# Performance work log

Measured on AMD Instinct MI355X. Metric: run time of the kernel, lower is better.

Reference implementation:

```python
import jax, jax.numpy as jnp
import numpy as np

L, DIN, D, NL = 16384, 256, 768, 8
EPS = 1e-5


def _ln(x, g, b):
    mu = jnp.mean(x, axis=-1, keepdims=True)
    var = jnp.mean(jnp.square(x - mu), axis=-1, keepdims=True)
    return (x - mu) * jax.lax.rsqrt(var + EPS) * g + b


def setup_inputs() -> dict:
    key = jax.random.key(0)
    ks = iter(jax.random.split(key, 24))
    nrm = lambda shape, s=0.02: jax.random.normal(next(ks), shape, jnp.float32) * s
    return {
        "node_features": jax.random.normal(next(ks), (L, DIN), jnp.float32),
        "W_proj": nrm((DIN, D)), "b_proj": jnp.zeros((D,), jnp.float32),
        "ln_s_g": jnp.ones((NL, D), jnp.float32), "ln_s_b": jnp.zeros((NL, D), jnp.float32),
        "W_in": nrm((NL, D, D)), "b_in": jnp.zeros((NL, D), jnp.float32),
        "W_gate": nrm((NL, D, D)), "b_gate": jnp.zeros((NL, D), jnp.float32),
        "W_out": nrm((NL, D, D)), "b_out": jnp.zeros((NL, D), jnp.float32),
        "decay_logit": nrm((NL, D), 0.5),
        "ln_f_g": jnp.ones((NL, D), jnp.float32), "ln_f_b": jnp.zeros((NL, D), jnp.float32),
        "W_ff1": nrm((NL, D, 2 * D)), "b_ff1": jnp.zeros((NL, 2 * D), jnp.float32),
        "W_ff2": nrm((NL, 2 * D, D)), "b_ff2": jnp.zeros((NL, D), jnp.float32),
        "ln_o_g": jnp.ones((D,), jnp.float32), "ln_o_b": jnp.zeros((D,), jnp.float32),
    }


def reference(node_features, W_proj, b_proj, ln_s_g, ln_s_b, W_in, b_in,
              W_gate, b_gate, W_out, b_out, decay_logit, ln_f_g, ln_f_b,
              W_ff1, b_ff1, W_ff2, b_ff2, ln_o_g, ln_o_b):
    x = node_features @ W_proj + b_proj  # [L, D]
    for l in range(NL):
        h = _ln(x, ln_s_g[l], ln_s_b[l])
        u = h @ W_in[l] + b_in[l]                      # [L, D]
        gate = jax.nn.sigmoid(h @ W_gate[l] + b_gate[l])
        decay = jax.nn.sigmoid(decay_logit[l])         # [D]

        def step(state, u_t):
            state = decay * state + u_t
            return state, state

        _, states = jax.lax.scan(step, jnp.zeros((D,), x.dtype), u)  # [L, D]
        x = x + (states * gate) @ W_out[l] + b_out[l]
        hf = _ln(x, ln_f_g[l], ln_f_b[l])
        x = x + jax.nn.silu(hf @ W_ff1[l] + b_ff1[l]) @ W_ff2[l] + b_ff2[l]
    return _ln(x, ln_o_g, ln_o_b)
```

## Files before the change

kernel.cpp:

```cpp
#include <hip/hip_runtime.h>
#include <hip/hip_bf16.h>
#include <math.h>
#include <string.h>

#define L_TOK 16384
#define D_INP 256
#define D_MOD 768
#define D_FF  1536
#define N_LAYER 8
#define S_T 64
#define S_G 256
#define EPSV 1e-5f

typedef short bf16x8 __attribute__((ext_vector_type(8)));
typedef float f32x4 __attribute__((ext_vector_type(4)));
typedef __hip_bfloat16 bf16;
typedef unsigned int u32;
typedef unsigned short u16;

__device__ __forceinline__ float fsigmoid(float z) { return 1.0f / (1.0f + __expf(-z)); }

__device__ __forceinline__ u16 f2bf(float f) {
  __hip_bfloat16 h = __float2bfloat16(f);
  u16 r; memcpy(&r, &h, 2); return r;
}
__device__ __forceinline__ float bf2f(u16 v) {
  u32 x = ((u32)v) << 16; float f; memcpy(&f, &x, 4); return f;
}

__device__ __forceinline__ void glds16(const short* g, short* l) {
  __builtin_amdgcn_global_load_lds(
      (const __attribute__((address_space(1))) unsigned int*)(g),
      (__attribute__((address_space(3))) unsigned int*)(l), 16, 0, 0);
}

__global__ void k_f32_to_bf16v(const float4* __restrict__ src, ushort4* __restrict__ dst, int n4) {
  int i = blockIdx.x * blockDim.x + threadIdx.x;
  if (i < n4) {
    float4 v = src[i];
    ushort4 o; o.x = f2bf(v.x); o.y = f2bf(v.y); o.z = f2bf(v.z); o.w = f2bf(v.w);
    dst[i] = o;
  }
}

template<bool FOLD>
__global__ void k_transpose_fold(const float* __restrict__ src, bf16* __restrict__ dst,
                                 int R, int C, size_t sstride, size_t dstride,
                                 const float* __restrict__ gv, const float* __restrict__ bv,
                                 float* __restrict__ wacc, float* __restrict__ bacc,
                                 int vstride) {
  __shared__ float tile[32][33];
  int z = blockIdx.z;
  const float* s = src + (size_t)z * sstride;
  bf16* d = dst + (size_t)z * dstride;
  int r0 = blockIdx.y * 32, c0 = blockIdx.x * 32;
  int tx = threadIdx.x, ty = threadIdx.y;
#pragma unroll
  for (int i = ty; i < 32; i += 8)
    tile[i][tx] = s[(size_t)(r0 + i) * C + (c0 + tx)];
  __syncthreads();
  float gk = 1.0f;
  if (FOLD) gk = gv[(size_t)z * R + r0 + tx];
#pragma unroll
  for (int i = ty; i < 32; i += 8) {
    float val = tile[tx][i];
    if (FOLD) val *= gk;
    d[(size_t)(c0 + i) * R + (r0 + tx)] = __float2bfloat16(val);
  }
  if (FOLD && ty == 0) {
    const float* gz = gv + (size_t)z * R + r0;
    const float* bz = bv + (size_t)z * R + r0;
    float s1 = 0.f, s2 = 0.f;
#pragma unroll 8
    for (int j = 0; j < 32; j++) {
      float wv = tile[j][tx];
      s1 += gz[j] * wv;
      s2 += bz[j] * wv;
    }
    atomicAdd(&wacc[(size_t)z * vstride + c0 + tx], s1);
    atomicAdd(&bacc[(size_t)z * vstride + c0 + tx], s2);
  }
}

template<int MODE, bool LNFOLD, bool STATS>
__global__ __launch_bounds__(256, 4) void k_gemm128(
    const short* __restrict__ A, const short* __restrict__ Bt,
    const float* __restrict__ bias, const float* __restrict__ bias2,
    const float* __restrict__ wvec, const float* __restrict__ bvec,
    const float* __restrict__ stats_in, float* __restrict__ stats_out,
    u16* __restrict__ res, u16* __restrict__ outp, u16* __restrict__ outp2,
    int N, int K, int ncol)
{
  __shared__ short As[2][128 * 32];
  __shared__ short Bs[2][128 * 32];
  __shared__ float s_mu[128], s_rv[128];
  const int tid = threadIdx.x;
  const int lane = tid & 63, w = tid >> 6;
  const int wr = w >> 1, wc = w & 1;
  const int l16 = lane & 15, qd = lane >> 4;

  const int b = blockIdx.x;
  const int xcd = b & 7, t = b >> 3;
  const int m0 = (xcd * 16 + t / ncol) * 128;
  const int n0 = (t % ncol) * 128;

  const int sr = lane >> 2, sc = lane & 3;
  const int ar = w * 32 + sr;
  const int acx = sc ^ ((ar >> 1) & 3);
  const short* ag0 = A  + (size_t)(m0 + ar) * K + acx * 8;
  const short* ag1 = ag0 + (size_t)16 * K;
  const short* bg0 = Bt + (size_t)(n0 + ar) * K + acx * 8;
  const short* bg1 = bg0 + (size_t)16 * K;

  const int fo = (qd ^ ((l16 >> 1) & 3)) * 8 + l16 * 32;

  f32x4 acc[4][4];
#pragma unroll
  for (int i = 0; i < 4; i++)
#pragma unroll
    for (int j = 0; j < 4; j++) acc[i][j] = (f32x4){0.f, 0.f, 0.f, 0.f};

  {
    short* a0 = &As[0][w * 1024];
    glds16(ag0, a0); glds16(ag1, a0 + 512);
    short* b0 = &Bs[0][w * 1024];
    glds16(bg0, b0); glds16(bg1, b0 + 512);
  }
  if (LNFOLD && tid < 128) {
    float sv  = stats_in[2 * (m0 + tid)];
    float sq  = stats_in[2 * (m0 + tid) + 1];
    float mu  = sv * (1.0f / (float)D_MOD);
    float var = sq * (1.0f / (float)D_MOD) - mu * mu;
    s_mu[tid] = mu;
    s_rv[tid] = 1.0f / sqrtf(var + EPSV);
  }
  int p = 0;
  for (int k0 = 0; k0 < K; k0 += 32, p ^= 1) {
    __syncthreads();
    if (k0 + 32 < K) {
      short* a0 = &As[p ^ 1][w * 1024];
      glds16(ag0 + k0 + 32, a0); glds16(ag1 + k0 + 32, a0 + 512);
      short* b0 = &Bs[p ^ 1][w * 1024];
      glds16(bg0 + k0 + 32, b0); glds16(bg1 + k0 + 32, b0 + 512);
    }
    const short* afb = &As[p][wr * 2048 + fo];
    const short* bfb = &Bs[p][wc * 2048 + fo];
    bf16x8 af[4], bfr[4];
#pragma unroll
    for (int rt = 0; rt < 4; rt++) af[rt] = *(const bf16x8*)(afb + rt * 512);
#pragma unroll
    for (int ct = 0; ct < 4; ct++) bfr[ct] = *(const bf16x8*)(bfb + ct * 512);
#pragma unroll
    for (int rt = 0; rt < 4; rt++)
#pragma unroll
      for (int ct = 0; ct < 4; ct++)
        acc[rt][ct] = __builtin_amdgcn_mfma_f32_16x16x32_bf16(af[rt], bfr[ct], acc[rt][ct], 0, 0, 0);
  }

  const float* bb = bias;
  u16* op = outp;
  int nofs = 0, Nout = N;
  bool sig = false;
  if (MODE == 4) {
    Nout = N >> 1;
    if (n0 >= Nout) { bb = bias2; op = outp2; nofs = Nout; sig = true; }
  }
  const int gmb = m0 + wr * 64 + qd * 4;
  const int gnb = n0 + wc * 64 + l16;
  float bc[4], wv4[4], bv4[4];
#pragma unroll
  for (int ct = 0; ct < 4; ct++) {
    int gn = gnb + ct * 16;
    bc[ct] = bb[gn - nofs];
    if (LNFOLD) { wv4[ct] = wvec[gn]; bv4[ct] = bvec[gn]; }
  }
#pragma unroll
  for (int rt = 0; rt < 4; rt++) {
#pragma unroll
    for (int r = 0; r < 4; r++) {
      const int gm = gmb + rt * 16 + r;
      float mu = 0.f, rv = 0.f;
      if (LNFOLD) { mu = s_mu[gm - m0]; rv = s_rv[gm - m0]; }
      float ps = 0.f, ps2 = 0.f;
#pragma unroll
      for (int ct = 0; ct < 4; ct++) {
        int gn = gnb + ct * 16;
        float vv = acc[rt][ct][r];
        if (LNFOLD) vv = rv * vv - rv * mu * wv4[ct] + bv4[ct] + bc[ct];
        else        vv += bc[ct];
        if (MODE == 2) vv = vv * fsigmoid(vv);
        if (MODE == 4 && sig) vv = fsigmoid(vv);
        size_t oidx = (size_t)gm * Nout + (gn - nofs);
        if (MODE == 3) vv += bf2f(res[oidx]);
        u16 rb = f2bf(vv);
        op[oidx] = rb;
        if (STATS) { float fv = bf2f(rb); ps += fv; ps2 += fv * fv; }
      }
      if (STATS) {
#pragma unroll
        for (int o = 1; o < 16; o <<= 1) {
          ps  += __shfl_xor(ps, o, 64);
          ps2 += __shfl_xor(ps2, o, 64);
        }
        if (l16 == 0) {
          atomicAdd(&stats_out[2 * gm], ps);
          atomicAdd(&stats_out[2 * gm + 1], ps2);
        }
      }
    }
  }
}

__global__ void k_scan_a(const bf16* __restrict__ u, const float* __restrict__ dl,
                         float* __restrict__ clast) {
  int t = threadIdx.x;
  int g = blockIdx.x;
  int d0 = t * 4;
  float dec[4], s[4] = {0.f, 0.f, 0.f, 0.f};
#pragma unroll
  for (int c = 0; c < 4; c++) dec[c] = fsigmoid(dl[d0 + c]);
  const ushort4* up = (const ushort4*)(u + (size_t)g * S_T * D_MOD) + t;
  for (int tt = 0; tt < S_T; tt++) {
    ushort4 uv = up[(size_t)tt * 192];
    s[0] = fmaf(dec[0], s[0], bf2f(uv.x));
    s[1] = fmaf(dec[1], s[1], bf2f(uv.y));
    s[2] = fmaf(dec[2], s[2], bf2f(uv.z));
    s[3] = fmaf(dec[3], s[3], bf2f(uv.w));
  }
#pragma unroll
  for (int c = 0; c < 4; c++) clast[(size_t)g * D_MOD + d0 + c] = s[c];
}

__global__ void k_scan_b(const float* __restrict__ clast, const float* __restrict__ dl,
                         float* __restrict__ carry) {
  int d = threadIdx.x;
  float decay = fsigmoid(dl[d]);
  float aT = decay;
#pragma unroll
  for (int i = 0; i < 6; i++) aT *= aT;
  float c = 0.f;
  for (int g = 0; g < S_G; g++) {
    carry[(size_t)g * D_MOD + d] = c;
    c = fmaf(aT, c, clast[(size_t)g * D_MOD + d]);
  }
}

__global__ void k_scan_c(const bf16* __restrict__ u, const float* __restrict__ dl,
                         const float* __restrict__ carry, bf16* __restrict__ gate_s) {
  int t = threadIdx.x;
  int g = blockIdx.x;
  int d0 = t * 4;
  float dec[4], s[4];
#pragma unroll
  for (int c = 0; c < 4; c++) {
    dec[c] = fsigmoid(dl[d0 + c]);
    s[c] = carry[(size_t)g * D_MOD + d0 + c];
  }
  const ushort4* up = (const ushort4*)(u + (size_t)g * S_T * D_MOD) + t;
  ushort4* gp = (ushort4*)(gate_s + (size_t)g * S_T * D_MOD) + t;
  for (int tt = 0; tt < S_T; tt++) {
    ushort4 uv = up[(size_t)tt * 192];
    ushort4 gv = gp[(size_t)tt * 192];
    s[0] = fmaf(dec[0], s[0], bf2f(uv.x));
    s[1] = fmaf(dec[1], s[1], bf2f(uv.y));
    s[2] = fmaf(dec[2], s[2], bf2f(uv.z));
    s[3] = fmaf(dec[3], s[3], bf2f(uv.w));
    ushort4 ov;
    ov.x = f2bf(s[0] * bf2f(gv.x));
    ov.y = f2bf(s[1] * bf2f(gv.y));
    ov.z = f2bf(s[2] * bf2f(gv.z));
    ov.w = f2bf(s[3] * bf2f(gv.w));
    gp[(size_t)tt * 192] = ov;
  }
}

__global__ __launch_bounds__(256) void k_ln_final(const u16* __restrict__ x,
    const float* __restrict__ stats, const float* __restrict__ g,
    const float* __restrict__ b, float* __restrict__ outp) {
  int wv = threadIdx.x >> 6, lane = threadIdx.x & 63;
  int row = blockIdx.x * 4 + wv;
  float sv = stats[2 * row], sq = stats[2 * row + 1];
  float mu = sv * (1.0f / (float)D_MOD);
  float var = sq * (1.0f / (float)D_MOD) - mu * mu;
  float rv = 1.0f / sqrtf(var + EPSV);
  const ushort4* xr = (const ushort4*)(x + (size_t)row * D_MOD);
  const float4* g4 = (const float4*)g;
  const float4* b4 = (const float4*)b;
  float4* o4 = (float4*)(outp + (size_t)row * D_MOD);
#pragma unroll
  for (int j = 0; j < 3; j++) {
    int f = j * 64 + lane;
    ushort4 xv = xr[f];
    float4 gg = g4[f], bb = b4[f], ov;
    ov.x = (bf2f(xv.x) - mu) * rv * gg.x + bb.x;
    ov.y = (bf2f(xv.y) - mu) * rv * gg.y + bb.y;
    ov.z = (bf2f(xv.z) - mu) * rv * gg.z + bb.z;
    ov.w = (bf2f(xv.w) - mu) * rv * gg.w + bb.w;
    o4[f] = ov;
  }
}

extern "C" void kernel_launch(void* const* d_in, const int* in_sizes, int n_in,
                              void* d_out, int out_size, void* d_ws, size_t ws_size,
                              hipStream_t stream) {
  const float* nf     = (const float*)d_in[0];
  const float* W_proj = (const float*)d_in[1];
  const float* b_proj = (const float*)d_in[2];
  const float* ln_s_g = (const float*)d_in[3];
  const float* ln_s_b = (const float*)d_in[4];
  const float* W_in   = (const float*)d_in[5];
  const float* b_in   = (const float*)d_in[6];
  const float* W_gate = (const float*)d_in[7];
  const float* b_gate = (const float*)d_in[8];
  const float* W_out  = (const float*)d_in[9];
  const float* b_out  = (const float*)d_in[10];
  const float* dlogit = (const float*)d_in[11];
  const float* ln_f_g = (const float*)d_in[12];
  const float* ln_f_b = (const float*)d_in[13];
  const float* W_ff1  = (const float*)d_in[14];
  const float* b_ff1  = (const float*)d_in[15];
  const float* W_ff2  = (const float*)d_in[16];
  const float* b_ff2  = (const float*)d_in[17];
  const float* ln_o_g = (const float*)d_in[18];
  const float* ln_o_b = (const float*)d_in[19];
  (void)in_sizes; (void)n_in;

  char* ws = (char*)d_ws;
  size_t off = 0;
  auto alloc = [&](size_t bytes) -> char* {
    char* p = ws + off;
    off = (off + bytes + 255) & ~(size_t)255;
    return p;
  };
  const bool big = ws_size >= (160ull << 20);
  const size_t wmul = big ? N_LAYER : 1;

  u16*   x     = (u16*)alloc(2ull * L_TOK * D_MOD);
  char*  ug    = alloc(2ull * L_TOK * D_FF);
  u16*   u     = (u16*)ug;
  u16*   gate  = (u16*)(ug + 2ull * L_TOK * D_MOD);
  u16*   tb    = (u16*)ug;
  u16*   nfb   = (u16*)ug;
  bf16*  WprojT= (bf16*)alloc(2ull * D_INP * D_MOD);
  bf16*  WigT  = (bf16*)alloc(2ull * wmul * (2 * D_MOD) * D_MOD);
  bf16*  WoT   = (bf16*)alloc(2ull * wmul * D_MOD * D_MOD);
  bf16*  Wff1T = (bf16*)alloc(2ull * wmul * D_MOD * D_FF);
  bf16*  Wff2T = (bf16*)alloc(2ull * wmul * D_FF * D_MOD);
  float* clast = (float*)alloc(sizeof(float) * (size_t)S_G * D_MOD);
  float* carry = (float*)alloc(sizeof(float) * (size_t)S_G * D_MOD);
  char*  zbase = alloc(0);
  float* stats = (float*)alloc(sizeof(float) * 17ull * L_TOK * 2);
  float* wvig  = (float*)alloc(sizeof(float) * N_LAYER * 2 * D_MOD);
  float* bvig  = (float*)alloc(sizeof(float) * N_LAYER * 2 * D_MOD);
  float* wvf1  = (float*)alloc(sizeof(float) * N_LAYER * D_FF);
  float* bvf1  = (float*)alloc(sizeof(float) * N_LAYER * D_FF);
  size_t zbytes = (size_t)((char*)ws + off - zbase);
  hipMemsetAsync(zbase, 0, zbytes, stream);

  const size_t DD = (size_t)D_MOD * D_MOD, DF = (size_t)D_MOD * D_FF;
  auto statslot = [&](int s) { return stats + (size_t)s * L_TOK * 2; };
  dim3 tb32(32, 8);
  k_f32_to_bf16v<<<(L_TOK * D_INP / 4 + 255) / 256, 256, 0, stream>>>(
      (const float4*)nf, (ushort4*)nfb, L_TOK * D_INP / 4);
  k_transpose_fold<false><<<dim3(D_MOD / 32, D_INP / 32, 1), tb32, 0, stream>>>(
      W_proj, WprojT, D_INP, D_MOD, 0, 0, nullptr, nullptr, nullptr, nullptr, 0);
  if (big) {
    k_transpose_fold<true><<<dim3(D_MOD / 32, D_MOD / 32, N_LAYER), tb32, 0, stream>>>(
        W_in,   WigT,      D_MOD, D_MOD, DD, 2 * DD, ln_s_g, ln_s_b, wvig,       bvig,       2 * D_MOD);
    k_transpose_fold<true><<<dim3(D_MOD / 32, D_MOD / 32, N_LAYER), tb32, 0, stream>>>(
        W_gate, WigT + DD, D_MOD, D_MOD, DD, 2 * DD, ln_s_g, ln_s_b, wvig + D_MOD, bvig + D_MOD, 2 * D_MOD);
    k_transpose_fold<false><<<dim3(D_MOD / 32, D_MOD / 32, N_LAYER), tb32, 0, stream>>>(
        W_out,  WoT,       D_MOD, D_MOD, DD, DD, nullptr, nullptr, nullptr, nullptr, 0);
    k_transpose_fold<true><<<dim3(D_FF / 32,  D_MOD / 32, N_LAYER), tb32, 0, stream>>>(
        W_ff1,  Wff1T,     D_MOD, D_FF,  DF, DF, ln_f_g, ln_f_b, wvf1, bvf1, D_FF);
    k_transpose_fold<false><<<dim3(D_MOD / 32, D_FF / 32,  N_LAYER), tb32, 0, stream>>>(
        W_ff2,  Wff2T,     D_FF,  D_MOD, DF, DF, nullptr, nullptr, nullptr, nullptr, 0);
  }

  k_gemm128<0, false, true><<<128 * 6, 256, 0, stream>>>(
      (const short*)nfb, (const short*)WprojT, b_proj, nullptr, nullptr, nullptr,
      nullptr, statslot(0), nullptr, x, nullptr, D_MOD, D_INP, 6);

  for (int l = 0; l < N_LAYER; l++) {
    const bf16 *wigT, *woT, *wf1T, *wf2T;
    if (big) {
      wigT = WigT  + (size_t)l * 2 * DD;
      woT  = WoT   + (size_t)l * DD;
      wf1T = Wff1T + (size_t)l * DF;
      wf2T = Wff2T + (size_t)l * DF;
    } else {
      k_transpose_fold<true><<<dim3(D_MOD / 32, D_MOD / 32, 1), tb32, 0, stream>>>(
          W_in + (size_t)l * DD, WigT, D_MOD, D_MOD, 0, 0,
          ln_s_g + l * D_MOD, ln_s_b + l * D_MOD, wvig + (size_t)l * 2 * D_MOD, bvig + (size_t)l * 2 * D_MOD, 0);
      k_transpose_fold<true><<<dim3(D_MOD / 32, D_MOD / 32, 1), tb32, 0, stream>>>(
          W_gate + (size_t)l * DD, WigT + DD, D_MOD, D_MOD, 0, 0,
          ln_s_g + l * D_MOD, ln_s_b + l * D_MOD, wvig + (size_t)l * 2 * D_MOD + D_MOD, bvig + (size_t)l * 2 * D_MOD + D_MOD, 0);
      k_transpose_fold<false><<<dim3(D_MOD / 32, D_MOD / 32, 1), tb32, 0, stream>>>(
          W_out + (size_t)l * DD, WoT, D_MOD, D_MOD, 0, 0, nullptr, nullptr, nullptr, nullptr, 0);
      k_transpose_fold<true><<<dim3(D_FF / 32, D_MOD / 32, 1), tb32, 0, stream>>>(
          W_ff1 + (size_t)l * DF, Wff1T, D_MOD, D_FF, 0, 0,
          ln_f_g + l * D_MOD, ln_f_b + l * D_MOD, wvf1 + (size_t)l * D_FF, bvf1 + (size_t)l * D_FF, 0);
      k_transpose_fold<false><<<dim3(D_MOD / 32, D_FF / 32, 1), tb32, 0, stream>>>(
          W_ff2 + (size_t)l * DF, Wff2T, D_FF, D_MOD, 0, 0, nullptr, nullptr, nullptr, nullptr, 0);
      wigT = WigT; woT = WoT; wf1T = Wff1T; wf2T = Wff2T;
    }

    k_gemm128<4, true, false><<<128 * 12, 256, 0, stream>>>(
        (const short*)x, (const short*)wigT, b_in + l * D_MOD, b_gate + l * D_MOD,
        wvig + (size_t)l * 2 * D_MOD, bvig + (size_t)l * 2 * D_MOD,
        statslot(2 * l), nullptr, nullptr, u, gate, 2 * D_MOD, D_MOD, 12);
    k_scan_a<<<S_G, 192, 0, stream>>>((const bf16*)u, dlogit + l * D_MOD, clast);
    k_scan_b<<<1, D_MOD, 0, stream>>>(clast, dlogit + l * D_MOD, carry);
    k_scan_c<<<S_G, 192, 0, stream>>>((const bf16*)u, dlogit + l * D_MOD, carry, (bf16*)gate);
    k_gemm128<3, false, true><<<128 * 6, 256, 0, stream>>>(
        (const short*)gate, (const short*)woT, b_out + l * D_MOD, nullptr, nullptr, nullptr,
        nullptr, statslot(2 * l + 1), x, x, nullptr, D_MOD, D_MOD, 6);
    k_gemm128<2, true, false><<<128 * 12, 256, 0, stream>>>(
        (const short*)x, (const short*)wf1T, b_ff1 + l * D_FF, nullptr,
        wvf1 + (size_t)l * D_FF, bvf1 + (size_t)l * D_FF,
        statslot(2 * l + 1), nullptr, nullptr, tb, nullptr, D_FF, D_MOD, 12);
    k_gemm128<3, false, true><<<128 * 6, 256, 0, stream>>>(
        (const short*)tb, (const short*)wf2T, b_ff2 + l * D_MOD, nullptr, nullptr, nullptr,
        nullptr, statslot(2 * l + 2), x, x, nullptr, D_MOD, D_FF, 6);
  }

  k_ln_final<<<L_TOK / 4, 256, 0, stream>>>(x, statslot(2 * N_LAYER), ln_o_g, ln_o_b, (float*)d_out);
}
```

Measured before the change: 2.290 ms.

## Replace 128x128 GEMM with 256x256 tile, 8-wave ping-pong pipelined kernel

```diff
diff --git a/kernel.cpp b/kernel.cpp
--- a/kernel.cpp
+++ b/kernel.cpp
@@ -83,7 +83,7 @@
 }
 
 template<int MODE, bool LNFOLD, bool STATS>
-__global__ __launch_bounds__(256, 4) void k_gemm128(
+__global__ __launch_bounds__(512, 2) void k_gemm256(
     const short* __restrict__ A, const short* __restrict__ Bt,
     const float* __restrict__ bias, const float* __restrict__ bias2,
     const float* __restrict__ wvec, const float* __restrict__ bvec,
@@ -91,70 +91,133 @@
     u16* __restrict__ res, u16* __restrict__ outp, u16* __restrict__ outp2,
     int N, int K, int ncol)
 {
-  __shared__ short As[2][128 * 32];
-  __shared__ short Bs[2][128 * 32];
-  __shared__ float s_mu[128], s_rv[128];
+  __shared__ short As[4 * 8192];
+  __shared__ short Bs[4 * 8192];
+  __shared__ float s_mu[256], s_rv[256];
+
   const int tid = threadIdx.x;
   const int lane = tid & 63, w = tid >> 6;
-  const int wr = w >> 1, wc = w & 1;
+  const int wr = w >> 2, wc = w & 3;
   const int l16 = lane & 15, qd = lane >> 4;
 
   const int b = blockIdx.x;
-  const int xcd = b & 7, t = b >> 3;
-  const int m0 = (xcd * 16 + t / ncol) * 128;
-  const int n0 = (t % ncol) * 128;
-
-  const int sr = lane >> 2, sc = lane & 3;
-  const int ar = w * 32 + sr;
-  const int acx = sc ^ ((ar >> 1) & 3);
-  const short* ag0 = A  + (size_t)(m0 + ar) * K + acx * 8;
-  const short* ag1 = ag0 + (size_t)16 * K;
-  const short* bg0 = Bt + (size_t)(n0 + ar) * K + acx * 8;
-  const short* bg1 = bg0 + (size_t)16 * K;
-
-  const int fo = (qd ^ ((l16 >> 1) & 3)) * 8 + l16 * 32;
-
-  f32x4 acc[4][4];
-#pragma unroll
-  for (int i = 0; i < 4; i++)
-#pragma unroll
-    for (int j = 0; j < 4; j++) acc[i][j] = (f32x4){0.f, 0.f, 0.f, 0.f};
-
-  {
-    short* a0 = &As[0][w * 1024];
-    glds16(ag0, a0); glds16(ag1, a0 + 512);
-    short* b0 = &Bs[0][w * 1024];
-    glds16(bg0, b0); glds16(bg1, b0 + 512);
-  }
-  if (LNFOLD && tid < 128) {
-    float sv  = stats_in[2 * (m0 + tid)];
-    float sq  = stats_in[2 * (m0 + tid) + 1];
+  const int xcd = b & 7, tt = b >> 3;
+  const int m0 = (xcd * 8 + tt / ncol) * 256;
+  const int n0 = (tt % ncol) * 256;
+
+  const int srow  = w * 16 + (lane >> 2);
+  const int skoct = (lane & 3) ^ ((lane >> 3) & 3);
+  const short* pA0 = A  + (size_t)(m0 + srow) * K + skoct * 8;
+  const short* pA1 = pA0 + (size_t)128 * K;
+  const short* pB0 = Bt + (size_t)(n0 + srow) * K + skoct * 8;
+  const short* pB1 = pB0 + (size_t)128 * K;
+
+  auto stg = [&](short* region, const short* p0, const short* p1, int koff) {
+    glds16(p0 + koff, region + w * 512);
+    glds16(p1 + koff, region + 4096 + w * 512);
+  };
+
+  const int kx   = (qd ^ ((l16 >> 1) & 3)) << 4;
+  const int aoff = (wr * 128 + l16) * 64 + kx;
+  const int boff = (wc * 64  + l16) * 64 + kx;
+
+  float sv = 0.f, sq = 0.f;
+  if (LNFOLD && tid < 256) {
+    sv = stats_in[2 * (m0 + tid)];
+    sq = stats_in[2 * (m0 + tid) + 1];
+  }
+
+  const int NT = K >> 6;
+  stg(Bs + 0 * 8192, pB0, pB1, 0);
+  stg(As + 0 * 8192, pA0, pA1, 0);
+  stg(Bs + 1 * 8192, pB0, pB1, 32);
+  stg(As + 1 * 8192, pA0, pA1, 32);
+  stg(Bs + 2 * 8192, pB0, pB1, 64);
+  stg(As + 2 * 8192, pA0, pA1, 64);
+  stg(Bs + 3 * 8192, pB0, pB1, 96);
+
+  if (LNFOLD && tid < 256) {
     float mu  = sv * (1.0f / (float)D_MOD);
     float var = sq * (1.0f / (float)D_MOD) - mu * mu;
     s_mu[tid] = mu;
     s_rv[tid] = 1.0f / sqrtf(var + EPSV);
   }
-  int p = 0;
-  for (int k0 = 0; k0 < K; k0 += 32, p ^= 1) {
-    __syncthreads();
-    if (k0 + 32 < K) {
-      short* a0 = &As[p ^ 1][w * 1024];
-      glds16(ag0 + k0 + 32, a0); glds16(ag1 + k0 + 32, a0 + 512);
-      short* b0 = &Bs[p ^ 1][w * 1024];
-      glds16(bg0 + k0 + 32, b0); glds16(bg1 + k0 + 32, b0 + 512);
-    }
-    const short* afb = &As[p][wr * 2048 + fo];
-    const short* bfb = &Bs[p][wc * 2048 + fo];
-    bf16x8 af[4], bfr[4];
-#pragma unroll
-    for (int rt = 0; rt < 4; rt++) af[rt] = *(const bf16x8*)(afb + rt * 512);
-#pragma unroll
-    for (int ct = 0; ct < 4; ct++) bfr[ct] = *(const bf16x8*)(bfb + ct * 512);
-#pragma unroll
-    for (int rt = 0; rt < 4; rt++)
-#pragma unroll
-      for (int ct = 0; ct < 4; ct++)
-        acc[rt][ct] = __builtin_amdgcn_mfma_f32_16x16x32_bf16(af[rt], bfr[ct], acc[rt][ct], 0, 0, 0);
+
+  f32x4 acc[8][4];
+#pragma unroll
+  for (int i = 0; i < 8; i++)
+#pragma unroll
+    for (int j = 0; j < 4; j++) acc[i][j] = (f32x4){0.f, 0.f, 0.f, 0.f};
+
+  asm volatile("s_waitcnt vmcnt(6)" ::: "memory");
+  __builtin_amdgcn_s_barrier();
+
+  bf16x8 af[4], b0f[4], b1f[4];
+  int buf = 0;
+  for (int t = 0; t < NT; ++t, buf ^= 1) {
+    const char* Ak0 = (const char*)As + buf * 32768;
+    const char* Ak1 = Ak0 + 16384;
+    const char* Bk0 = (const char*)Bs + buf * 32768;
+    const char* Bk1 = Bk0 + 16384;
+    const int nb = buf ^ 1;
+
+    if (t + 1 < NT) stg(As + (nb * 2 + 1) * 8192, pA0, pA1, (t + 1) * 64 + 32);
+#pragma unroll
+    for (int i = 0; i < 4; i++) af[i]  = *(const bf16x8*)(Ak0 + aoff + i * 1024);
+#pragma unroll
+    for (int i = 0; i < 4; i++) b0f[i] = *(const bf16x8*)(Bk0 + boff + i * 1024);
+    __builtin_amdgcn_s_barrier();
+    __builtin_amdgcn_s_setprio(1);
+#pragma unroll
+    for (int rf = 0; rf < 4; rf++)
+#pragma unroll
+      for (int cf = 0; cf < 4; cf++)
+        acc[rf][cf] = __builtin_amdgcn_mfma_f32_16x16x32_bf16(af[rf], b0f[cf], acc[rf][cf], 0, 0, 0);
+    __builtin_amdgcn_s_setprio(0);
+    __builtin_amdgcn_s_barrier();
+
+    if (t + 2 < NT) stg(Bs + (buf * 2 + 0) * 8192, pB0, pB1, (t + 2) * 64);
+#pragma unroll
+    for (int i = 0; i < 4; i++) af[i] = *(const bf16x8*)(Ak0 + aoff + (4 + i) * 1024);
+    __builtin_amdgcn_s_barrier();
+    __builtin_amdgcn_s_setprio(1);
+#pragma unroll
+    for (int rf = 0; rf < 4; rf++)
+#pragma unroll
+      for (int cf = 0; cf < 4; cf++)
+        acc[4 + rf][cf] = __builtin_amdgcn_mfma_f32_16x16x32_bf16(af[rf], b0f[cf], acc[4 + rf][cf], 0, 0, 0);
+    __builtin_amdgcn_s_setprio(0);
+    __builtin_amdgcn_s_barrier();
+
+    if (t + 2 < NT) stg(As + (buf * 2 + 0) * 8192, pA0, pA1, (t + 2) * 64);
+#pragma unroll
+    for (int i = 0; i < 4; i++) af[i]  = *(const bf16x8*)(Ak1 + aoff + i * 1024);
+#pragma unroll
+    for (int i = 0; i < 4; i++) b1f[i] = *(const bf16x8*)(Bk1 + boff + i * 1024);
+    __builtin_amdgcn_s_barrier();
+    __builtin_amdgcn_s_setprio(1);
+#pragma unroll
+    for (int rf = 0; rf < 4; rf++)
+#pragma unroll
+      for (int cf = 0; cf < 4; cf++)
+        acc[rf][cf] = __builtin_amdgcn_mfma_f32_16x16x32_bf16(af[rf], b1f[cf], acc[rf][cf], 0, 0, 0);
+    __builtin_amdgcn_s_setprio(0);
+    __builtin_amdgcn_s_barrier();
+
+    if (t + 2 < NT) stg(Bs + (buf * 2 + 1) * 8192, pB0, pB1, (t + 2) * 64 + 32);
+#pragma unroll
+    for (int i = 0; i < 4; i++) af[i] = *(const bf16x8*)(Ak1 + aoff + (4 + i) * 1024);
+    __builtin_amdgcn_s_barrier();
+    __builtin_amdgcn_s_setprio(1);
+#pragma unroll
+    for (int rf = 0; rf < 4; rf++)
+#pragma unroll
+      for (int cf = 0; cf < 4; cf++)
+        acc[4 + rf][cf] = __builtin_amdgcn_mfma_f32_16x16x32_bf16(af[rf], b1f[cf], acc[4 + rf][cf], 0, 0, 0);
+    __builtin_amdgcn_s_setprio(0);
+    if (t + 2 < NT) asm volatile("s_waitcnt vmcnt(6)" ::: "memory");
+    else            asm volatile("s_waitcnt vmcnt(0)" ::: "memory");
+    __builtin_amdgcn_s_barrier();
   }
 
   const float* bb = bias;
@@ -165,29 +228,29 @@
     Nout = N >> 1;
     if (n0 >= Nout) { bb = bias2; op = outp2; nofs = Nout; sig = true; }
   }
-  const int gmb = m0 + wr * 64 + qd * 4;
+  const int gmb = m0 + wr * 128 + qd * 4;
   const int gnb = n0 + wc * 64 + l16;
   float bc[4], wv4[4], bv4[4];
 #pragma unroll
-  for (int ct = 0; ct < 4; ct++) {
-    int gn = gnb + ct * 16;
-    bc[ct] = bb[gn - nofs];
-    if (LNFOLD) { wv4[ct] = wvec[gn]; bv4[ct] = bvec[gn]; }
-  }
-#pragma unroll
-  for (int rt = 0; rt < 4; rt++) {
+  for (int cf = 0; cf < 4; cf++) {
+    int gn = gnb + cf * 16;
+    bc[cf] = bb[gn - nofs];
+    if (LNFOLD) { wv4[cf] = wvec[gn]; bv4[cf] = bvec[gn]; }
+  }
+#pragma unroll
+  for (int rf = 0; rf < 8; rf++) {
 #pragma unroll
     for (int r = 0; r < 4; r++) {
-      const int gm = gmb + rt * 16 + r;
+      const int gm = gmb + rf * 16 + r;
       float mu = 0.f, rv = 0.f;
       if (LNFOLD) { mu = s_mu[gm - m0]; rv = s_rv[gm - m0]; }
       float ps = 0.f, ps2 = 0.f;
 #pragma unroll
-      for (int ct = 0; ct < 4; ct++) {
-        int gn = gnb + ct * 16;
-        float vv = acc[rt][ct][r];
-        if (LNFOLD) vv = rv * vv - rv * mu * wv4[ct] + bv4[ct] + bc[ct];
-        else        vv += bc[ct];
+      for (int cf = 0; cf < 4; cf++) {
+        int gn = gnb + cf * 16;
+        float vv = acc[rf][cf][r];
+        if (LNFOLD) vv = rv * vv - rv * mu * wv4[cf] + bv4[cf] + bc[cf];
+        else        vv += bc[cf];
         if (MODE == 2) vv = vv * fsigmoid(vv);
         if (MODE == 4 && sig) vv = fsigmoid(vv);
         size_t oidx = (size_t)gm * Nout + (gn - nofs);
@@ -377,9 +440,9 @@
         W_ff2,  Wff2T,     D_FF,  D_MOD, DF, DF, nullptr, nullptr, nullptr, nullptr, 0);
   }
 
-  k_gemm128<0, false, true><<<128 * 6, 256, 0, stream>>>(
+  k_gemm256<0, false, true><<<64 * 3, 512, 0, stream>>>(
       (const short*)nfb, (const short*)WprojT, b_proj, nullptr, nullptr, nullptr,
-      nullptr, statslot(0), nullptr, x, nullptr, D_MOD, D_INP, 6);
+      nullptr, statslot(0), nullptr, x, nullptr, D_MOD, D_INP, 3);
 
   for (int l = 0; l < N_LAYER; l++) {
     const bf16 *wigT, *woT, *wf1T, *wf2T;
@@ -405,23 +468,23 @@
       wigT = WigT; woT = WoT; wf1T = Wff1T; wf2T = Wff2T;
     }
 
-    k_gemm128<4, true, false><<<128 * 12, 256, 0, stream>>>(
+    k_gemm256<4, true, false><<<64 * 6, 512, 0, stream>>>(
         (const short*)x, (const short*)wigT, b_in + l * D_MOD, b_gate + l * D_MOD,
         wvig + (size_t)l * 2 * D_MOD, bvig + (size_t)l * 2 * D_MOD,
-        statslot(2 * l), nullptr, nullptr, u, gate, 2 * D_MOD, D_MOD, 12);
+        statslot(2 * l), nullptr, nullptr, u, gate, 2 * D_MOD, D_MOD, 6);
     k_scan_a<<<S_G, 192, 0, stream>>>((const bf16*)u, dlogit + l * D_MOD, clast);
     k_scan_b<<<1, D_MOD, 0, stream>>>(clast, dlogit + l * D_MOD, carry);
     k_scan_c<<<S_G, 192, 0, stream>>>((const bf16*)u, dlogit + l * D_MOD, carry, (bf16*)gate);
-    k_gemm128<3, false, true><<<128 * 6, 256, 0, stream>>>(
+    k_gemm256<3, false, true><<<64 * 3, 512, 0, stream>>>(
         (const short*)gate, (const short*)woT, b_out + l * D_MOD, nullptr, nullptr, nullptr,
-        nullptr, statslot(2 * l + 1), x, x, nullptr, D_MOD, D_MOD, 6);
-    k_gemm128<2, true, false><<<128 * 12, 256, 0, stream>>>(
+        nullptr, statslot(2 * l + 1), x, x, nullptr, D_MOD, D_MOD, 3);
+    k_gemm256<2, true, false><<<64 * 6, 512, 0, stream>>>(
         (const short*)x, (const short*)wf1T, b_ff1 + l * D_FF, nullptr,
         wvf1 + (size_t)l * D_FF, bvf1 + (size_t)l * D_FF,
-        statslot(2 * l + 1), nullptr, nullptr, tb, nullptr, D_FF, D_MOD, 12);
-    k_gemm128<3, false, true><<<128 * 6, 256, 0, stream>>>(
+        statslot(2 * l + 1), nullptr, nullptr, tb, nullptr, D_FF, D_MOD, 6);
+    k_gemm256<3, false, true><<<64 * 3, 512, 0, stream>>>(
         (const short*)tb, (const short*)wf2T, b_ff2 + l * D_MOD, nullptr, nullptr, nullptr,
-        nullptr, statslot(2 * l + 2), x, x, nullptr, D_MOD, D_FF, 6);
+        nullptr, statslot(2 * l + 2), x, x, nullptr, D_MOD, D_FF, 3);
   }
 
   k_ln_final<<<L_TOK / 4, 256, 0, stream>>>(x, statslot(2 * N_LAYER), ln_o_g, ln_o_b, (float*)d_out);
```

Result: slower. 2.598 ms (+13.4%).

## Triple-buffer GEMM LDS staging with manual waitcnt and inline ds_read

Applied to the files above, without the earlier changes.

```diff
diff --git a/kernel.cpp b/kernel.cpp
--- a/kernel.cpp
+++ b/kernel.cpp
@@ -32,6 +32,14 @@
   __builtin_amdgcn_global_load_lds(
       (const __attribute__((address_space(1))) unsigned int*)(g),
       (__attribute__((address_space(3))) unsigned int*)(l), 16, 0, 0);
+}
+
+__device__ __forceinline__ bf16x8 dsr128(const char* base, int imm) {
+  bf16x8 r;
+  const __attribute__((address_space(3))) char* p =
+      (const __attribute__((address_space(3))) char*)base;
+  asm volatile("ds_read_b128 %0, %1 offset:%c2" : "=v"(r) : "v"(p), "i"(imm));
+  return r;
 }
 
 __global__ void k_f32_to_bf16v(const float4* __restrict__ src, ushort4* __restrict__ dst, int n4) {
@@ -91,8 +99,8 @@
     u16* __restrict__ res, u16* __restrict__ outp, u16* __restrict__ outp2,
     int N, int K, int ncol)
 {
-  __shared__ short As[2][128 * 32];
-  __shared__ short Bs[2][128 * 32];
+  __shared__ short As[3][128 * 32];
+  __shared__ short Bs[3][128 * 32];
   __shared__ float s_mu[128], s_rv[128];
   const int tid = threadIdx.x;
   const int lane = tid & 63, w = tid >> 6;
@@ -112,49 +120,66 @@
   const short* bg0 = Bt + (size_t)(n0 + ar) * K + acx * 8;
   const short* bg1 = bg0 + (size_t)16 * K;
 
+  auto stg = [&](int bi, int k0) {
+    short* a0 = &As[bi][w * 1024];
+    glds16(ag0 + k0, a0); glds16(ag1 + k0, a0 + 512);
+    short* b0 = &Bs[bi][w * 1024];
+    glds16(bg0 + k0, b0); glds16(bg1 + k0, b0 + 512);
+  };
+
   const int fo = (qd ^ ((l16 >> 1) & 3)) * 8 + l16 * 32;
 
-  f32x4 acc[4][4];
-#pragma unroll
-  for (int i = 0; i < 4; i++)
-#pragma unroll
-    for (int j = 0; j < 4; j++) acc[i][j] = (f32x4){0.f, 0.f, 0.f, 0.f};
-
-  {
-    short* a0 = &As[0][w * 1024];
-    glds16(ag0, a0); glds16(ag1, a0 + 512);
-    short* b0 = &Bs[0][w * 1024];
-    glds16(bg0, b0); glds16(bg1, b0 + 512);
-  }
+  float sv = 0.f, sq = 0.f;
   if (LNFOLD && tid < 128) {
-    float sv  = stats_in[2 * (m0 + tid)];
-    float sq  = stats_in[2 * (m0 + tid) + 1];
+    sv = stats_in[2 * (m0 + tid)];
+    sq = stats_in[2 * (m0 + tid) + 1];
+  }
+
+  const int NT = K >> 5;
+  stg(0, 0);
+  stg(1, 32);
+
+  if (LNFOLD && tid < 128) {
     float mu  = sv * (1.0f / (float)D_MOD);
     float var = sq * (1.0f / (float)D_MOD) - mu * mu;
     s_mu[tid] = mu;
     s_rv[tid] = 1.0f / sqrtf(var + EPSV);
   }
-  int p = 0;
-  for (int k0 = 0; k0 < K; k0 += 32, p ^= 1) {
-    __syncthreads();
-    if (k0 + 32 < K) {
-      short* a0 = &As[p ^ 1][w * 1024];
-      glds16(ag0 + k0 + 32, a0); glds16(ag1 + k0 + 32, a0 + 512);
-      short* b0 = &Bs[p ^ 1][w * 1024];
-      glds16(bg0 + k0 + 32, b0); glds16(bg1 + k0 + 32, b0 + 512);
+
+  f32x4 acc[4][4];
+#pragma unroll
+  for (int i = 0; i < 4; i++)
+#pragma unroll
+    for (int j = 0; j < 4; j++) acc[i][j] = (f32x4){0.f, 0.f, 0.f, 0.f};
+
+  asm volatile("s_waitcnt vmcnt(4)" ::: "memory");
+  __builtin_amdgcn_s_barrier();
+
+  int rd = 0;
+  for (int t2 = 0; t2 < NT; ++t2) {
+    const char* ab = (const char*)&As[rd][wr * 2048 + fo];
+    const char* bb = (const char*)&Bs[rd][wc * 2048 + fo];
+    bf16x8 af0 = dsr128(ab, 0),    af1 = dsr128(ab, 1024);
+    bf16x8 af2 = dsr128(ab, 2048), af3 = dsr128(ab, 3072);
+    bf16x8 bf0 = dsr128(bb, 0),    bf1 = dsr128(bb, 1024);
+    bf16x8 bf2 = dsr128(bb, 2048), bf3 = dsr128(bb, 3072);
+    if (t2 + 2 < NT) {
+      int st = (rd == 0) ? 2 : rd - 1;
+      stg(st, (t2 + 2) * 32);
     }
-    const short* afb = &As[p][wr * 2048 + fo];
-    const short* bfb = &Bs[p][wc * 2048 + fo];
-    bf16x8 af[4], bfr[4];
-#pragma unroll
-    for (int rt = 0; rt < 4; rt++) af[rt] = *(const bf16x8*)(afb + rt * 512);
-#pragma unroll
-    for (int ct = 0; ct < 4; ct++) bfr[ct] = *(const bf16x8*)(bfb + ct * 512);
+    asm volatile("s_waitcnt lgkmcnt(0)" ::: "memory");
+    __builtin_amdgcn_sched_barrier(0);
+    bf16x8 af[4] = {af0, af1, af2, af3};
+    bf16x8 bfr[4] = {bf0, bf1, bf2, bf3};
 #pragma unroll
     for (int rt = 0; rt < 4; rt++)
 #pragma unroll
       for (int ct = 0; ct < 4; ct++)
         acc[rt][ct] = __builtin_amdgcn_mfma_f32_16x16x32_bf16(af[rt], bfr[ct], acc[rt][ct], 0, 0, 0);
+    if (t2 + 2 < NT) asm volatile("s_waitcnt vmcnt(4)" ::: "memory");
+    else             asm volatile("s_waitcnt vmcnt(0)" ::: "memory");
+    __builtin_amdgcn_s_barrier();
+    rd = (rd == 2) ? 0 : rd + 1;
   }
 
   const float* bb = bias;
```

Result: no change. 2.305 ms (+0.6%).
